# Performance work log

Measured on AMD Instinct MI355X. Metric: run time of the kernel, lower is better.

Reference implementation:

```python
import jax, jax.numpy as jnp
import numpy as np


def _affine_matrix(params):
    # params: [N,5] = (theta, scale_x, scale_y, tx, ty)
    theta, sx, sy, tx, ty = (params[:, i] for i in range(5))
    a = sx * jnp.cos(theta)
    b = -jnp.sin(theta)
    c = tx
    d = jnp.sin(theta)
    e = sy * jnp.cos(theta)
    f = ty
    return jnp.stack([a, b, c, d, e, f], axis=-1).reshape(-1, 2, 3)


def _forward(x, params, small_h, small_w):
    N, C, H, W = x.shape
    A = _affine_matrix(params)  # [N,2,3]
    # nearest-downsample of the full-res affine grid == evaluating the affine
    # map at the nearest-sampled base coordinates (src = floor(dst * in/out))
    ws = jnp.floor(jnp.arange(small_w) * (W / small_w)).astype(jnp.int32)
    hs = jnp.floor(jnp.arange(small_h) * (H / small_h)).astype(jnp.int32)
    # base normalized coords of F.affine_grid with align_corners=False
    gx = (2.0 * ws.astype(x.dtype) + 1.0) / W - 1.0  # [Ws]
    gy = (2.0 * hs.astype(x.dtype) + 1.0) / H - 1.0  # [Hs]
    bx = jnp.broadcast_to(gx[None, :], (small_h, small_w))
    by = jnp.broadcast_to(gy[:, None], (small_h, small_w))
    # apply affine per batch: [N,Hs,Ws]
    sx_ = A[:, 0, 0, None, None] * bx + A[:, 0, 1, None, None] * by + A[:, 0, 2, None, None]
    sy_ = A[:, 1, 0, None, None] * bx + A[:, 1, 1, None, None] * by + A[:, 1, 2, None, None]
    # grid_sample: bilinear, padding_mode='zeros', align_corners=False
    ix = ((sx_ + 1.0) * W - 1.0) * 0.5
    iy = ((sy_ + 1.0) * H - 1.0) * 0.5
    x0 = jnp.floor(ix)
    y0 = jnp.floor(iy)
    x1 = x0 + 1.0
    y1 = y0 + 1.0
    wx1 = ix - x0
    wx0 = 1.0 - wx1
    wy1 = iy - y0
    wy0 = 1.0 - wy1

    def gather(img, yi, xi):
        # img: [C,H,W]; yi, xi: [Hs,Ws] float pixel indices
        valid = (xi >= 0) & (xi <= W - 1) & (yi >= 0) & (yi <= H - 1)
        xc = jnp.clip(xi, 0, W - 1).astype(jnp.int32)
        yc = jnp.clip(yi, 0, H - 1).astype(jnp.int32)
        v = img[:, yc, xc]  # [C,Hs,Ws]
        return v * valid[None].astype(img.dtype)

    def sample_one(img, x0, x1, y0, y1, wx0, wx1, wy0, wy1):
        return (gather(img, y0, x0) * (wy0 * wx0)[None]
                + gather(img, y0, x1) * (wy0 * wx1)[None]
                + gather(img, y1, x0) * (wy1 * wx0)[None]
                + gather(img, y1, x1) * (wy1 * wx1)[None])

    return jax.vmap(sample_one)(x, x0, x1, y0, y1, wx0, wx1, wy0, wy1)


def setup_inputs() -> dict:
    key = jax.random.key(0)
    k1, k2 = jax.random.split(key)
    x = jax.random.normal(k1, (16, 32, 512, 512), dtype=jnp.float32)
    params = jax.random.uniform(k2, (16, 5), dtype=jnp.float32)
    return {"x": x, "params": params, "small_h": 256, "small_w": 256}


def reference(x, params, small_h, small_w):
    return _forward(x, params, small_h, small_w)
```

## Files before the change

kernel.cpp:

```cpp
#include <hip/hip_runtime.h>

constexpr int N_  = 16;
constexpr int C_  = 32;
constexpr int H_  = 512;
constexpr int W_  = 512;
constexpr int SH_ = 256;
constexpr int SW_ = 256;

constexpr int LDSH = 50;
constexpr int LDSW = 50;
constexpr int LDSS = 51;

__device__ __forceinline__ float src_coord(float ca, float cb, float cbias,
                                           int wk, int hk) {
    const float gx = (2.0f * (float)(2 * wk) + 1.0f) * (1.0f / (float)W_) - 1.0f;
    const float gy = (2.0f * (float)(2 * hk) + 1.0f) * (1.0f / (float)H_) - 1.0f;
    const float s  = ca * gx + cb * gy + cbias;
    return ((s + 1.0f) * (float)W_ - 1.0f) * 0.5f;
}

__global__ __launch_bounds__(256) void affine_sample_kernel(
    const float* __restrict__ x,
    const float* __restrict__ params,
    float* __restrict__ out)
{
    __shared__ float tile[LDSH * LDSS];

    const int lx = threadIdx.x;
    const int ly = threadIdx.y;
    const int w  = blockIdx.x * 16 + lx;
    const int h  = blockIdx.y * 16 + ly;
    const int n  = blockIdx.z;

    const float theta = params[n * 5 + 0];
    const float psx   = params[n * 5 + 1];
    const float psy   = params[n * 5 + 2];
    const float ptx   = params[n * 5 + 3];
    const float pty   = params[n * 5 + 4];
    const float st = sinf(theta);
    const float ct = cosf(theta);
    const float a = psx * ct, b = -st,      cc = ptx;
    const float d = st,       e = psy * ct, f  = pty;

    const float ix = src_coord(a, b, cc, w, h);
    const float iy = src_coord(d, e, f,  w, h);

    const float x0f = floorf(ix);
    const float y0f = floorf(iy);
    const float x1f = x0f + 1.0f;
    const float y1f = y0f + 1.0f;
    const float wx1 = ix - x0f, wx0 = 1.0f - wx1;
    const float wy1 = iy - y0f, wy0 = 1.0f - wy1;

    const float vx0 = (x0f >= 0.0f && x0f <= (float)(W_ - 1)) ? 1.0f : 0.0f;
    const float vx1 = (x1f >= 0.0f && x1f <= (float)(W_ - 1)) ? 1.0f : 0.0f;
    const float vy0 = (y0f >= 0.0f && y0f <= (float)(H_ - 1)) ? 1.0f : 0.0f;
    const float vy1 = (y1f >= 0.0f && y1f <= (float)(H_ - 1)) ? 1.0f : 0.0f;

    const float w00 = wy0 * wx0 * vy0 * vx0;
    const float w01 = wy0 * wx1 * vy0 * vx1;
    const float w10 = wy1 * wx0 * vy1 * vx0;
    const float w11 = wy1 * wx1 * vy1 * vx1;

    const int x0i = (int)x0f, y0i = (int)y0f;
    const int x0c = min(max(x0i,     0), W_ - 1);
    const int x1c = min(max(x0i + 1, 0), W_ - 1);
    const int y0c = min(max(y0i,     0), H_ - 1);
    const int y1c = min(max(y0i + 1, 0), H_ - 1);

    const int w0 = blockIdx.x * 16, w1 = w0 + 15;
    const int h0 = blockIdx.y * 16, h1 = h0 + 15;
    const float cx00 = src_coord(a, b, cc, w0, h0);
    const float cx10 = src_coord(a, b, cc, w1, h0);
    const float cx01 = src_coord(a, b, cc, w0, h1);
    const float cx11 = src_coord(a, b, cc, w1, h1);
    const float cy00 = src_coord(d, e, f,  w0, h0);
    const float cy10 = src_coord(d, e, f,  w1, h0);
    const float cy01 = src_coord(d, e, f,  w0, h1);
    const float cy11 = src_coord(d, e, f,  w1, h1);
    const float ixmin = fminf(fminf(cx00, cx10), fminf(cx01, cx11));
    const float ixmax = fmaxf(fmaxf(cx00, cx10), fmaxf(cx01, cx11));
    const float iymin = fminf(fminf(cy00, cy10), fminf(cy01, cy11));
    const float iymax = fmaxf(fmaxf(cy00, cy10), fmaxf(cy01, cy11));

    int xlo = (int)floorf(ixmin) - 1, xhi = (int)floorf(ixmax) + 2;
    int ylo = (int)floorf(iymin) - 1, yhi = (int)floorf(iymax) + 2;
    xlo = min(max(xlo, 0), W_ - 1);  xhi = min(max(xhi, 0), W_ - 1);
    ylo = min(max(ylo, 0), H_ - 1);  yhi = min(max(yhi, 0), H_ - 1);
    const int bw = xhi - xlo + 1;
    const int bh = yhi - ylo + 1;

    const float* __restrict__ p = x + (size_t)n * C_ * H_ * W_;
    float* __restrict__ o = out + (((size_t)n * C_) * SH_ + h) * SW_ + w;

    if (bw <= LDSW && bh <= LDSH) {
        const int l00 = (y0c - ylo) * LDSS + (x0c - xlo);
        const int l01 = (y0c - ylo) * LDSS + (x1c - xlo);
        const int l10 = (y1c - ylo) * LDSS + (x0c - xlo);
        const int l11 = (y1c - ylo) * LDSS + (x1c - xlo);

        const float* __restrict__ ps = p + ylo * W_ + xlo;
#pragma unroll 1
        for (int ch = 0; ch < C_; ++ch) {
            __syncthreads();
            for (int r = ly; r < bh; r += 16)
                for (int cx = lx; cx < bw; cx += 16)
                    tile[r * LDSS + cx] = ps[r * W_ + cx];
            __syncthreads();
            const float v00 = tile[l00];
            const float v01 = tile[l01];
            const float v10 = tile[l10];
            const float v11 = tile[l11];
            *o = v00 * w00 + v01 * w01 + v10 * w10 + v11 * w11;
            ps += H_ * W_;
            o  += SH_ * SW_;
        }
    } else {
        const int off00 = y0c * W_ + x0c;
        const int off01 = y0c * W_ + x1c;
        const int off10 = y1c * W_ + x0c;
        const int off11 = y1c * W_ + x1c;
#pragma unroll 8
        for (int ch = 0; ch < C_; ++ch) {
            const float v00 = p[off00];
            const float v01 = p[off01];
            const float v10 = p[off10];
            const float v11 = p[off11];
            *o = v00 * w00 + v01 * w01 + v10 * w10 + v11 * w11;
            p += H_ * W_;
            o += SH_ * SW_;
        }
    }
}

extern "C" void kernel_launch(void* const* d_in, const int* in_sizes, int n_in,
                              void* d_out, int out_size, void* d_ws, size_t ws_size,
                              hipStream_t stream) {
    const float* x      = (const float*)d_in[0];
    const float* params = (const float*)d_in[1];
    float* out = (float*)d_out;

    dim3 block(16, 16, 1);
    dim3 grid(SW_ / 16, SH_ / 16, N_);
    affine_sample_kernel<<<grid, block, 0, stream>>>(x, params, out);
}
```

Before: 881.5 us.

## Stage fixed 48x64 tiles with float4 loads, two channels per step, register prefetch

Replaces the variable-size scalar LDS fill with a fixed 48x64 window loaded as float4 per thread. Each step handles two channels at once, and the next pair is prefetched into registers while the current pair is sampled from LDS. This removes the per-element loop overhead, halves the barrier count, and overlaps global loads with compute. The cost is loading a fixed window even when the footprint is smaller, more registers, and a window narrower than before (61 columns usable) that may send more blocks to the direct-gather path.

```diff
diff --git a/kernel.cpp b/kernel.cpp
--- a/kernel.cpp
+++ b/kernel.cpp
@@ -7,9 +7,9 @@
 constexpr int SH_ = 256;
 constexpr int SW_ = 256;
 
-constexpr int LDSH = 50;
-constexpr int LDSW = 50;
-constexpr int LDSS = 51;
+constexpr int RH = 48;
+constexpr int RW = 64;
+constexpr int RS = 68;
 
 __device__ __forceinline__ float src_coord(float ca, float cb, float cbias,
                                            int wk, int hk) {
@@ -24,7 +24,7 @@
     const float* __restrict__ params,
     float* __restrict__ out)
 {
-    __shared__ float tile[LDSH * LDSS];
+    __shared__ float tile[2][RH * RS];
 
     const int lx = threadIdx.x;
     const int ly = threadIdx.y;
@@ -93,42 +93,72 @@
     const float* __restrict__ p = x + (size_t)n * C_ * H_ * W_;
     float* __restrict__ o = out + (((size_t)n * C_) * SH_ + h) * SW_ + w;
 
-    if (bw <= LDSW && bh <= LDSH) {
-        const int l00 = (y0c - ylo) * LDSS + (x0c - xlo);
-        const int l01 = (y0c - ylo) * LDSS + (x1c - xlo);
-        const int l10 = (y1c - ylo) * LDSS + (x0c - xlo);
-        const int l11 = (y1c - ylo) * LDSS + (x1c - xlo);
+    if (bw <= RW - 3 && bh <= RH) {
+        const int xstart = min(xlo & ~3, W_ - RW);
+        const int ystart = min(ylo, H_ - RH);
 
-        const float* __restrict__ ps = p + ylo * W_ + xlo;
-#pragma unroll 1
-        for (int ch = 0; ch < C_; ++ch) {
+        const int l00 = (y0c - ystart) * RS + (x0c - xstart);
+        const int l01 = (y0c - ystart) * RS + (x1c - xstart);
+        const int l10 = (y1c - ystart) * RS + (x0c - xstart);
+        const int l11 = (y1c - ystart) * RS + (x1c - xstart);
+
+        const int tid = ly * 16 + lx;
+        const int q  = (tid & 15) * 4;
+        const int r0 = tid >> 4;
+
+        const float* __restrict__ g = p + (size_t)ystart * W_ + xstart;
+        const size_t chs = (size_t)H_ * W_;
+
+        float4 va0 = *(const float4*)(g + (size_t)(r0     ) * W_ + q);
+        float4 va1 = *(const float4*)(g + (size_t)(r0 + 16) * W_ + q);
+        float4 va2 = *(const float4*)(g + (size_t)(r0 + 32) * W_ + q);
+        float4 vb0 = *(const float4*)(g + chs + (size_t)(r0     ) * W_ + q);
+        float4 vb1 = *(const float4*)(g + chs + (size_t)(r0 + 16) * W_ + q);
+        float4 vb2 = *(const float4*)(g + chs + (size_t)(r0 + 32) * W_ + q);
+
+        for (int ch = 0; ch < C_; ch += 2) {
             __syncthreads();
-            for (int r = ly; r < bh; r += 16)
-                for (int cx = lx; cx < bw; cx += 16)
-                    tile[r * LDSS + cx] = ps[r * W_ + cx];
+            *(float4*)(&tile[0][(r0     ) * RS + q]) = va0;
+            *(float4*)(&tile[0][(r0 + 16) * RS + q]) = va1;
+            *(float4*)(&tile[0][(r0 + 32) * RS + q]) = va2;
+            *(float4*)(&tile[1][(r0     ) * RS + q]) = vb0;
+            *(float4*)(&tile[1][(r0 + 16) * RS + q]) = vb1;
+            *(float4*)(&tile[1][(r0 + 32) * RS + q]) = vb2;
             __syncthreads();
-            const float v00 = tile[l00];
-            const float v01 = tile[l01];
-            const float v10 = tile[l10];
-            const float v11 = tile[l11];
-            *o = v00 * w00 + v01 * w01 + v10 * w10 + v11 * w11;
-            ps += H_ * W_;
-            o  += SH_ * SW_;
+
+            if (ch + 2 < C_) {
+                g += 2 * chs;
+                va0 = *(const float4*)(g + (size_t)(r0     ) * W_ + q);
+                va1 = *(const float4*)(g + (size_t)(r0 + 16) * W_ + q);
+                va2 = *(const float4*)(g + (size_t)(r0 + 32) * W_ + q);
+                vb0 = *(const float4*)(g + chs + (size_t)(r0     ) * W_ + q);
+                vb1 = *(const float4*)(g + chs + (size_t)(r0 + 16) * W_ + q);
+                vb2 = *(const float4*)(g + chs + (size_t)(r0 + 32) * W_ + q);
+            }
+
+            const float s0 = tile[0][l00] * w00 + tile[0][l01] * w01
+                           + tile[0][l10] * w10 + tile[0][l11] * w11;
+            const float s1 = tile[1][l00] * w00 + tile[1][l01] * w01
+                           + tile[1][l10] * w10 + tile[1][l11] * w11;
+            o[0]                   = s0;
+            o[(size_t)SH_ * SW_]   = s1;
+            o += 2 * (size_t)SH_ * SW_;
         }
     } else {
         const int off00 = y0c * W_ + x0c;
         const int off01 = y0c * W_ + x1c;
         const int off10 = y1c * W_ + x0c;
         const int off11 = y1c * W_ + x1c;
+        const float* __restrict__ pf = p;
 #pragma unroll 8
         for (int ch = 0; ch < C_; ++ch) {
-            const float v00 = p[off00];
-            const float v01 = p[off01];
-            const float v10 = p[off10];
-            const float v11 = p[off11];
+            const float v00 = pf[off00];
+            const float v01 = pf[off01];
+            const float v10 = pf[off10];
+            const float v11 = pf[off11];
             *o = v00 * w00 + v01 * w01 + v10 * w10 + v11 * w11;
-            p += H_ * W_;
-            o += SH_ * SW_;
+            pf += (size_t)H_ * W_;
+            o  += (size_t)SH_ * SW_;
         }
     }
 }
```

New measurement: 772.4 us. 12.4% less time.
